# Performance work log

Measured on AMD Instinct MI355X. Metric: run time of the kernel, lower is better.

The kernel has to match this reference:

```python
import jax, jax.numpy as jnp
import numpy as np

N, E, R, D, DEPTH = 50000, 800000, 1000, 128, 2


def setup_inputs() -> dict:
    key = jax.random.key(0)
    ks = jax.random.split(key, 6)
    features = jax.random.normal(ks[0], (N, D), jnp.float32)
    rel_emb = jax.random.normal(ks[1], (R, D), jnp.float32)
    # adj coalesced by row (torch coalesce sorts indices; values stay aligned)
    src = jnp.sort(jax.random.randint(ks[2], (E,), 0, N))
    dst = jax.random.randint(ks[3], (E,), 0, N)
    adj = jnp.stack([src, dst]).astype(jnp.int64)
    # one relation per triple: row index = triple id, col = relation id
    r_index = jnp.stack([jnp.arange(E), jax.random.randint(ks[4], (E,), 0, R)]).astype(jnp.int64)
    r_val = jax.random.uniform(ks[5], (E,), jnp.float32)
    attn_kernels = jax.random.normal(jax.random.fold_in(key, 7), (DEPTH, D), jnp.float32) * 0.1
    return {"features": features, "rel_emb": rel_emb, "adj": adj, "r_index": r_index,
            "r_val": r_val, "triple_size": E, "rel_size": R, "node_size": N,
            "attn_kernels": attn_kernels}


def _layer(features, rel_emb, adj, r_index, r_val, triple_size, node_size, attn_k):
    row = adj[0]
    neighs = features[adj[1]]                                   # [E, D] gather
    # sparse.mm(tri_rel, rel_emb): sum_j r_val * rel_emb[col] per triple row
    tri_rel = jax.ops.segment_sum(r_val[:, None] * rel_emb[r_index[1]],
                                  r_index[0], num_segments=triple_size)  # [E, D]
    nrm = jnp.linalg.norm(tri_rel, axis=1, keepdims=True)
    tri_rel = tri_rel / jnp.maximum(nrm, 1e-12)                 # F.normalize(p=2)
    # Householder-style reflection
    neighs = neighs - 2.0 * jnp.sum(neighs * tri_rel, axis=1, keepdims=True) * tri_rel
    att = tri_rel @ attn_k                                      # [E]
    # sparse row-wise softmax over edges grouped by destination row
    m = jax.ops.segment_max(att, row, num_segments=node_size)
    e = jnp.exp(att - m[row])
    s = jax.ops.segment_sum(e, row, num_segments=node_size)
    att = e / s[row]
    new_features = jax.ops.segment_sum(neighs * att[:, None], row,
                                       num_segments=node_size)  # [N, D] scatter
    return jnp.tanh(new_features)


def reference(features, rel_emb, adj, r_index, r_val, triple_size, rel_size, node_size, attn_kernels):
    features = jnp.tanh(features)
    outputs = [features]
    for l in range(attn_kernels.shape[0]):
        features = _layer(features, rel_emb, adj, r_index, r_val,
                          triple_size, node_size, attn_kernels[l])
        outputs.append(features)
    return jnp.concatenate(outputs, axis=-1)                    # [N, D*(depth+1)]
```

## Files before the change

### kernel.cpp

```cpp
#include <hip/hip_runtime.h>
#include <hip/hip_bf16.h>
#include <math.h>

#define N_NODES   50000
#define N_EDGES   800000
#define N_REL     1000
#define DIM       128
#define DEPTH_L   2
#define OUT_STRIDE (DIM * (DEPTH_L + 1))

#define TANH0_BLOCKS  ((N_NODES * 32) / 256)
#define EINFO_BLOCKS  ((N_EDGES + 255) / 256)

typedef _Float16 h2 __attribute__((ext_vector_type(2)));

#if defined(__has_builtin)
#if __has_builtin(__builtin_amdgcn_fdot2)
#define FDOT2(a, b, c) __builtin_amdgcn_fdot2((a), (b), (c), false)
#endif
#endif
#ifndef FDOT2
#define FDOT2(a, b, c) ((c) + (float)(a).x * (float)(b).x + (float)(a).y * (float)(b).y)
#endif

__device__ __forceinline__ float fast_tanh(float x) {
    float cx = fminf(fmaxf(x, -15.f), 15.f);
    float e = __expf(2.f * cx);
    return (e - 1.f) * __frcp_rn(e + 1.f);
}

__global__ __launch_bounds__(64) void prep_rel_kernel(
    const float* __restrict__ rel_emb,
    const float* __restrict__ attn_k,
    _Float16* __restrict__ rhat,
    float* __restrict__ er0, float* __restrict__ er1)
{
    int r = blockIdx.x;
    int lane = threadIdx.x;
    if (r == N_REL) {
        rhat[(size_t)r * DIM + lane]      = (_Float16)0.f;
        rhat[(size_t)r * DIM + lane + 64] = (_Float16)0.f;
        if (lane == 0) { er0[N_REL] = 1.f; er1[N_REL] = 1.f; }
        return;
    }
    float v0 = rel_emb[r * DIM + lane];
    float v1 = rel_emb[r * DIM + lane + 64];
    float ss = v0 * v0 + v1 * v1;
    #pragma unroll
    for (int o = 32; o >= 1; o >>= 1) ss += __shfl_xor(ss, o);
    float inv = 1.0f / fmaxf(sqrtf(ss), 1e-12f);
    float t0 = v0 * inv, t1 = v1 * inv;
    rhat[(size_t)r * DIM + lane]      = (_Float16)t0;
    rhat[(size_t)r * DIM + lane + 64] = (_Float16)t1;
    #pragma unroll
    for (int l = 0; l < DEPTH_L; ++l) {
        float d = t0 * attn_k[l * DIM + lane] + t1 * attn_k[l * DIM + lane + 64];
        #pragma unroll
        for (int o = 32; o >= 1; o >>= 1) d += __shfl_xor(d, o);
        if (lane == 0) {
            if (l == 0) er0[r] = __expf(d); else er1[r] = __expf(d);
        }
    }
}

__global__ __launch_bounds__(256) void rowptr_kernel(
    const int* __restrict__ src, int* __restrict__ rp,
    float* __restrict__ s0, float* __restrict__ s1)
{
    int n = blockIdx.x * blockDim.x + threadIdx.x;
    if (n > N_NODES) return;
    int lo = 0, hi = N_EDGES;
    while (lo < hi) {
        int mid = (lo + hi) >> 1;
        if (src[mid] < n) lo = mid + 1; else hi = mid;
    }
    rp[n] = lo;
    if (n < N_NODES) { s0[n] = 0.f; s1[n] = 0.f; }
}

__global__ __launch_bounds__(256) void aux_fused_kernel(
    const float* __restrict__ feat, float* __restrict__ out,
    _Float16* __restrict__ fs0,
    const int* __restrict__ src, const int* __restrict__ dst,
    const int* __restrict__ relid, const float* __restrict__ rval,
    const float* __restrict__ er0, const float* __restrict__ er1,
    float* __restrict__ s0, float* __restrict__ s1,
    uint2* __restrict__ einfo2)
{
    if (blockIdx.x < TANH0_BLOCKS) {
        int i = blockIdx.x * 256 + threadIdx.x;
        int n = i >> 5;
        int j = i & 31;
        float4 v = reinterpret_cast<const float4*>(feat + (size_t)n * DIM)[j];
        float4 o;
        o.x = fast_tanh(v.x); o.y = fast_tanh(v.y);
        o.z = fast_tanh(v.z); o.w = fast_tanh(v.w);
        reinterpret_cast<float4*>(out + (size_t)n * OUT_STRIDE)[j] = o;
        h2 p0; p0.x = (_Float16)o.x; p0.y = (_Float16)o.y;
        h2 p1; p1.x = (_Float16)o.z; p1.y = (_Float16)o.w;
        uint2 u;
        u.x = __builtin_bit_cast(unsigned, p0);
        u.y = __builtin_bit_cast(unsigned, p1);
        reinterpret_cast<uint2*>(fs0 + (size_t)n * DIM)[j] = u;
        return;
    }

    int e = (blockIdx.x - TANH0_BLOCKS) * 256 + threadIdx.x;
    if (e >= N_EDGES) return;
    int lane = threadIdx.x & 63;
    int sn = src[e];
    int r = (rval[e] == 0.f) ? N_REL : relid[e];
    float x0 = er0[r], x1 = er1[r];

    h2 ep; ep.x = (_Float16)x0; ep.y = (_Float16)x1;
    einfo2[e] = make_uint2((unsigned)dst[e] | ((unsigned)r << 16),
                           __builtin_bit_cast(unsigned, ep));

    #pragma unroll
    for (int off = 1; off < 64; off <<= 1) {
        float y0 = __shfl_up(x0, off);
        float y1 = __shfl_up(x1, off);
        int   sp = __shfl_up(sn, off);
        if (lane >= off && sp == sn) { x0 += y0; x1 += y1; }
    }
    int snext = __shfl_down(sn, 1);
    bool lastlane = (lane == 63) || (e == N_EDGES - 1) || (snext != sn);
    if (lastlane) {
        atomicAdd(&s0[sn], x0);
        atomicAdd(&s1[sn], x1);
    }
}

template<int L>
__global__ __launch_bounds__(128) void layer_fused_kernel(
    const _Float16* __restrict__ fs_in,
    float* __restrict__ fout,
    _Float16* __restrict__ fs_out,
    const uint2* __restrict__ einfo2,
    const int* __restrict__ rp,
    const float* __restrict__ s_l,
    const _Float16* __restrict__ rhat)
{
    int wid  = threadIdx.x >> 6;
    int lane = threadIdx.x & 63;
    int node = blockIdx.x * 2 + wid;
    if (node >= N_NODES) return;
    int start = rp[node], end = rp[node + 1];
    int g = lane >> 3;
    int q = lane & 7;

    float inv_s = 1.0f / s_l[node];

    const char* fbase = (const char*)fs_in + 32 * q;
    const char* tbase = (const char*)rhat  + 32 * q;
    int g0 = (lane >> 3) & 1, g1 = (lane >> 4) & 1, g2 = (lane >> 5) & 1;

    h2 a2[8];
    #pragma unroll
    for (int i = 0; i < 8; ++i) { a2[i].x = (_Float16)0.f; a2[i].y = (_Float16)0.f; }

    if (start < end) {
        int deg = end - start;
        bool small = (deg <= 64);
        unsigned eix = 0, eiy = 0;
        if (small) {
            int lc = start + lane; if (lc > end - 1) lc = end - 1;
            uint2 et = einfo2[lc];
            eix = et.x; eiy = et.y;
        }

        auto LOADC = [&](int e0, uint4& h0, uint4& h1, uint4& t0, uint4& t1,
                         float& w) {
            unsigned ax, ay;
            if (small) {
                int slot = e0 - start + g;
                ax = __shfl(eix, slot);
                ay = __shfl(eiy, slot);
            } else {
                int ec = e0 + g; if (ec > end - 1) ec = end - 1;
                uint2 et = einfo2[ec];
                ax = et.x; ay = et.y;
            }
            bool valid = (e0 + g < end);
            h0 = make_uint4(0u, 0u, 0u, 0u); h1 = h0; t0 = h0; t1 = h0;
            if (valid) {
                unsigned dn = ax & 0xffffu, rl = ax >> 16;
                const uint4* hp = reinterpret_cast<const uint4*>(fbase + (size_t)dn * 256);
                const uint4* tp = reinterpret_cast<const uint4*>(tbase + (size_t)rl * 256);
                h0 = hp[0]; h1 = hp[1];
                t0 = tp[0]; t1 = tp[1];
            }
            h2 ep = __builtin_bit_cast(h2, ay);
            float er = (float)((L == 0) ? ep.x : ep.y);
            w = valid ? er * inv_s : 0.f;
        };

        auto COMPUTEC = [&](uint4 h0, uint4 h1, uint4 t0, uint4 t1, float wf) {
            h2 hh[8], tt[8];
            hh[0] = __builtin_bit_cast(h2, h0.x); hh[1] = __builtin_bit_cast(h2, h0.y);
            hh[2] = __builtin_bit_cast(h2, h0.z); hh[3] = __builtin_bit_cast(h2, h0.w);
            hh[4] = __builtin_bit_cast(h2, h1.x); hh[5] = __builtin_bit_cast(h2, h1.y);
            hh[6] = __builtin_bit_cast(h2, h1.z); hh[7] = __builtin_bit_cast(h2, h1.w);
            tt[0] = __builtin_bit_cast(h2, t0.x); tt[1] = __builtin_bit_cast(h2, t0.y);
            tt[2] = __builtin_bit_cast(h2, t0.z); tt[3] = __builtin_bit_cast(h2, t0.w);
            tt[4] = __builtin_bit_cast(h2, t1.x); tt[5] = __builtin_bit_cast(h2, t1.y);
            tt[6] = __builtin_bit_cast(h2, t1.z); tt[7] = __builtin_bit_cast(h2, t1.w);
            float d0 = 0.f, d1 = 0.f;
            #pragma unroll
            for (int p = 0; p < 8; p += 2) {
                d0 = FDOT2(hh[p],     tt[p],     d0);
                d1 = FDOT2(hh[p + 1], tt[p + 1], d1);
            }
            float d = d0 + d1;
            d += __shfl_xor(d, 1);
            d += __shfl_xor(d, 2);
            d += __shfl_xor(d, 4);
            float cf = -2.f * wf * d;
            _Float16 wh  = (_Float16)wf;
            _Float16 cfh = (_Float16)cf;
            h2 wv; wv.x = wh;  wv.y = wh;
            h2 cv; cv.x = cfh; cv.y = cfh;
            #pragma unroll
            for (int p = 0; p < 8; ++p) {
                a2[p] = hh[p] * wv + a2[p];
                a2[p] = tt[p] * cv + a2[p];
            }
        };

        uint4 hA0, hA1, tA0, tA1; float wA;
        uint4 hB0, hB1, tB0, tB1; float wB;
        LOADC(start, hA0, hA1, tA0, tA1, wA);
        int e = start;
        while (true) {
            int e2 = e + 8;
            bool moreB = (e2 < end);
            if (moreB) LOADC(e2, hB0, hB1, tB0, tB1, wB);
            __builtin_amdgcn_sched_barrier(0);
            COMPUTEC(hA0, hA1, tA0, tA1, wA);
            e = e2;
            if (!moreB) break;
            int e3 = e + 8;
            bool moreA = (e3 < end);
            if (moreA) LOADC(e3, hA0, hA1, tA0, tA1, wA);
            __builtin_amdgcn_sched_barrier(0);
            COMPUTEC(hB0, hB1, tB0, tB1, wB);
            e = e3;
            if (!moreA) break;
        }
    }

    h2 b1[4];
    #pragma unroll
    for (int k = 0; k < 4; ++k) {
        h2 keep = g0 ? a2[2*k + 1] : a2[2*k];
        h2 send = g0 ? a2[2*k] : a2[2*k + 1];
        unsigned su = __shfl_xor(__builtin_bit_cast(unsigned, send), 8);
        b1[k] = keep + __builtin_bit_cast(h2, su);
    }
    h2 b2[2];
    #pragma unroll
    for (int m = 0; m < 2; ++m) {
        h2 keep = g1 ? b1[2*m + 1] : b1[2*m];
        h2 send = g1 ? b1[2*m] : b1[2*m + 1];
        unsigned su = __shfl_xor(__builtin_bit_cast(unsigned, send), 16);
        b2[m] = keep + __builtin_bit_cast(h2, su);
    }
    h2 c;
    {
        h2 keep = g2 ? b2[1] : b2[0];
        h2 send = g2 ? b2[0] : b2[1];
        unsigned su = __shfl_xor(__builtin_bit_cast(unsigned, send), 32);
        c = keep + __builtin_bit_cast(h2, su);
    }

    float y0 = fast_tanh((float)c.x), y1 = fast_tanh((float)c.y);
    int dimo = 16 * q + 2 * g;
    *reinterpret_cast<float2*>(fout + (size_t)node * OUT_STRIDE + dimo)
        = make_float2(y0, y1);
    if (L == 0) {
        h2 pr; pr.x = (_Float16)y0; pr.y = (_Float16)y1;
        *reinterpret_cast<h2*>(fs_out + (size_t)node * DIM + dimo) = pr;
    }
}

extern "C" void kernel_launch(void* const* d_in, const int* in_sizes, int n_in,
                              void* d_out, int out_size, void* d_ws, size_t ws_size,
                              hipStream_t stream)
{
    const float* features = (const float*)d_in[0];
    const float* rel_emb  = (const float*)d_in[1];
    const int*   adj      = (const int*)d_in[2];
    const int*   r_index  = (const int*)d_in[3];
    const float* r_val    = (const float*)d_in[4];
    const float* attn_k   = (const float*)d_in[8];
    float* out = (float*)d_out;

    const int* src   = adj;
    const int* dst   = adj + N_EDGES;
    const int* relid = r_index + N_EDGES;

    char* base = (char*)d_ws;
    _Float16* rhat = (_Float16*)base;
    float*    er0  = (float*)(base + 256256);
    float*    er1  = (float*)(base + 260264);
    int*      rp   = (int*)(base + 264272);
    float*    s0   = (float*)(base + 464288);
    float*    s1   = (float*)(base + 664288);
    uint2*    einfo2 = (uint2*)(base + 864288);
    _Float16* fs0  = (_Float16*)(base + 864288 + (size_t)N_EDGES * 8);
    _Float16* fs1  = fs0 + (size_t)N_NODES * DIM;

    prep_rel_kernel<<<N_REL + 1, 64, 0, stream>>>(rel_emb, attn_k, rhat, er0, er1);
    rowptr_kernel<<<(N_NODES + 1 + 255) / 256, 256, 0, stream>>>(src, rp, s0, s1);
    aux_fused_kernel<<<TANH0_BLOCKS + EINFO_BLOCKS, 256, 0, stream>>>(
        features, out, fs0, src, dst, relid, r_val, er0, er1, s0, s1, einfo2);

    layer_fused_kernel<0><<<(N_NODES + 1) / 2, 128, 0, stream>>>(
        fs0, out + 1 * DIM, fs1, einfo2, rp, s0, rhat);
    layer_fused_kernel<1><<<(N_NODES + 1) / 2, 128, 0, stream>>>(
        fs1, out + 2 * DIM, fs0, einfo2, rp, s1, rhat);
}
```

Baseline: 111.9 us.

## Process two nodes per wave in layer kernel and merge prep kernels

```diff
diff --git a/kernel.cpp b/kernel.cpp
--- a/kernel.cpp
+++ b/kernel.cpp
@@ -11,6 +11,8 @@
 
 #define TANH0_BLOCKS  ((N_NODES * 32) / 256)
 #define EINFO_BLOCKS  ((N_EDGES + 255) / 256)
+#define PREP_BLOCKS   ((N_REL + 1 + 3) / 4)
+#define RP_BLOCKS     ((N_NODES + 1 + 255) / 256)
 
 typedef _Float16 h2 __attribute__((ext_vector_type(2)));
 
@@ -29,45 +31,47 @@
     return (e - 1.f) * __frcp_rn(e + 1.f);
 }
 
-__global__ __launch_bounds__(64) void prep_rel_kernel(
+__global__ __launch_bounds__(256) void prep_kernel(
     const float* __restrict__ rel_emb,
     const float* __restrict__ attn_k,
     _Float16* __restrict__ rhat,
-    float* __restrict__ er0, float* __restrict__ er1)
-{
-    int r = blockIdx.x;
-    int lane = threadIdx.x;
-    if (r == N_REL) {
-        rhat[(size_t)r * DIM + lane]      = (_Float16)0.f;
-        rhat[(size_t)r * DIM + lane + 64] = (_Float16)0.f;
-        if (lane == 0) { er0[N_REL] = 1.f; er1[N_REL] = 1.f; }
-        return;
-    }
-    float v0 = rel_emb[r * DIM + lane];
-    float v1 = rel_emb[r * DIM + lane + 64];
-    float ss = v0 * v0 + v1 * v1;
-    #pragma unroll
-    for (int o = 32; o >= 1; o >>= 1) ss += __shfl_xor(ss, o);
-    float inv = 1.0f / fmaxf(sqrtf(ss), 1e-12f);
-    float t0 = v0 * inv, t1 = v1 * inv;
-    rhat[(size_t)r * DIM + lane]      = (_Float16)t0;
-    rhat[(size_t)r * DIM + lane + 64] = (_Float16)t1;
-    #pragma unroll
-    for (int l = 0; l < DEPTH_L; ++l) {
-        float d = t0 * attn_k[l * DIM + lane] + t1 * attn_k[l * DIM + lane + 64];
-        #pragma unroll
-        for (int o = 32; o >= 1; o >>= 1) d += __shfl_xor(d, o);
-        if (lane == 0) {
-            if (l == 0) er0[r] = __expf(d); else er1[r] = __expf(d);
-        }
-    }
-}
-
-__global__ __launch_bounds__(256) void rowptr_kernel(
+    float* __restrict__ er0, float* __restrict__ er1,
     const int* __restrict__ src, int* __restrict__ rp,
     float* __restrict__ s0, float* __restrict__ s1)
 {
-    int n = blockIdx.x * blockDim.x + threadIdx.x;
+    if (blockIdx.x < PREP_BLOCKS) {
+        int wid  = threadIdx.x >> 6;
+        int lane = threadIdx.x & 63;
+        int r = blockIdx.x * 4 + wid;
+        if (r > N_REL) return;
+        if (r == N_REL) {
+            rhat[(size_t)r * DIM + lane]      = (_Float16)0.f;
+            rhat[(size_t)r * DIM + lane + 64] = (_Float16)0.f;
+            if (lane == 0) { er0[N_REL] = 1.f; er1[N_REL] = 1.f; }
+            return;
+        }
+        float v0 = rel_emb[r * DIM + lane];
+        float v1 = rel_emb[r * DIM + lane + 64];
+        float ss = v0 * v0 + v1 * v1;
+        #pragma unroll
+        for (int o = 32; o >= 1; o >>= 1) ss += __shfl_xor(ss, o);
+        float inv = 1.0f / fmaxf(sqrtf(ss), 1e-12f);
+        float t0 = v0 * inv, t1 = v1 * inv;
+        rhat[(size_t)r * DIM + lane]      = (_Float16)t0;
+        rhat[(size_t)r * DIM + lane + 64] = (_Float16)t1;
+        #pragma unroll
+        for (int l = 0; l < DEPTH_L; ++l) {
+            float d = t0 * attn_k[l * DIM + lane] + t1 * attn_k[l * DIM + lane + 64];
+            #pragma unroll
+            for (int o = 32; o >= 1; o >>= 1) d += __shfl_xor(d, o);
+            if (lane == 0) {
+                if (l == 0) er0[r] = __expf(d); else er1[r] = __expf(d);
+            }
+        }
+        return;
+    }
+
+    int n = (blockIdx.x - PREP_BLOCKS) * 256 + threadIdx.x;
     if (n > N_NODES) return;
     int lo = 0, hi = N_EDGES;
     while (lo < hi) {
@@ -143,21 +147,27 @@
 {
     int wid  = threadIdx.x >> 6;
     int lane = threadIdx.x & 63;
-    int node = blockIdx.x * 2 + wid;
-    if (node >= N_NODES) return;
-    int start = rp[node], end = rp[node + 1];
+    int wave = blockIdx.x * 2 + wid;
+    int n0 = wave * 2;
+    if (n0 >= N_NODES) return;
+    int n1 = n0 + 1;
+    int start = rp[n0], mid = rp[n0 + 1], end = rp[n0 + 2];
+
+    float is0 = 1.0f / s_l[n0];
+    float is1 = 1.0f / s_l[n1];
+
     int g = lane >> 3;
     int q = lane & 7;
-
-    float inv_s = 1.0f / s_l[node];
-
     const char* fbase = (const char*)fs_in + 32 * q;
     const char* tbase = (const char*)rhat  + 32 * q;
     int g0 = (lane >> 3) & 1, g1 = (lane >> 4) & 1, g2 = (lane >> 5) & 1;
 
-    h2 a2[8];
+    h2 aA[8], aB[8];
     #pragma unroll
-    for (int i = 0; i < 8; ++i) { a2[i].x = (_Float16)0.f; a2[i].y = (_Float16)0.f; }
+    for (int i = 0; i < 8; ++i) {
+        aA[i].x = (_Float16)0.f; aA[i].y = (_Float16)0.f;
+        aB[i].x = (_Float16)0.f; aB[i].y = (_Float16)0.f;
+    }
 
     if (start < end) {
         int deg = end - start;
@@ -192,10 +202,25 @@
             }
             h2 ep = __builtin_bit_cast(h2, ay);
             float er = (float)((L == 0) ? ep.x : ep.y);
-            w = valid ? er * inv_s : 0.f;
+            float isv = (e0 + g >= mid) ? is1 : is0;
+            w = valid ? er * isv : 0.f;
         };
 
-        auto COMPUTEC = [&](uint4 h0, uint4 h1, uint4 t0, uint4 t1, float wf) {
+        auto ACC = [&](h2 (&acc)[8], float wf, float cf,
+                       const h2 (&hh)[8], const h2 (&tt)[8]) {
+            _Float16 wh  = (_Float16)wf;
+            _Float16 cfh = (_Float16)cf;
+            h2 wv; wv.x = wh;  wv.y = wh;
+            h2 cv; cv.x = cfh; cv.y = cfh;
+            #pragma unroll
+            for (int p = 0; p < 8; ++p) {
+                acc[p] = hh[p] * wv + acc[p];
+                acc[p] = tt[p] * cv + acc[p];
+            }
+        };
+
+        auto DOCHUNK = [&](int e0, uint4 h0, uint4 h1, uint4 t0, uint4 t1,
+                           float wf) {
             h2 hh[8], tt[8];
             hh[0] = __builtin_bit_cast(h2, h0.x); hh[1] = __builtin_bit_cast(h2, h0.y);
             hh[2] = __builtin_bit_cast(h2, h0.z); hh[3] = __builtin_bit_cast(h2, h0.w);
@@ -216,14 +241,18 @@
             d += __shfl_xor(d, 2);
             d += __shfl_xor(d, 4);
             float cf = -2.f * wf * d;
-            _Float16 wh  = (_Float16)wf;
-            _Float16 cfh = (_Float16)cf;
-            h2 wv; wv.x = wh;  wv.y = wh;
-            h2 cv; cv.x = cfh; cv.y = cfh;
-            #pragma unroll
-            for (int p = 0; p < 8; ++p) {
-                a2[p] = hh[p] * wv + a2[p];
-                a2[p] = tt[p] * cv + a2[p];
+
+            int realEnd = (e0 + 8 < end) ? (e0 + 8) : end;
+            if (realEnd <= mid) {
+                ACC(aA, wf, cf, hh, tt);
+            } else if (e0 >= mid) {
+                ACC(aB, wf, cf, hh, tt);
+            } else {
+                bool ma = (e0 + g < mid);
+                float wfa = ma ? wf : 0.f, cfa = ma ? cf : 0.f;
+                float wfb = ma ? 0.f : wf, cfb = ma ? 0.f : cf;
+                ACC(aA, wfa, cfa, hh, tt);
+                ACC(aB, wfb, cfb, hh, tt);
             }
         };
 
@@ -236,51 +265,54 @@
             bool moreB = (e2 < end);
             if (moreB) LOADC(e2, hB0, hB1, tB0, tB1, wB);
             __builtin_amdgcn_sched_barrier(0);
-            COMPUTEC(hA0, hA1, tA0, tA1, wA);
-            e = e2;
+            DOCHUNK(e, hA0, hA1, tA0, tA1, wA);
             if (!moreB) break;
-            int e3 = e + 8;
+            int e3 = e2 + 8;
             bool moreA = (e3 < end);
             if (moreA) LOADC(e3, hA0, hA1, tA0, tA1, wA);
             __builtin_amdgcn_sched_barrier(0);
-            COMPUTEC(hB0, hB1, tB0, tB1, wB);
+            DOCHUNK(e2, hB0, hB1, tB0, tB1, wB);
             e = e3;
             if (!moreA) break;
         }
     }
 
-    h2 b1[4];
-    #pragma unroll
-    for (int k = 0; k < 4; ++k) {
-        h2 keep = g0 ? a2[2*k + 1] : a2[2*k];
-        h2 send = g0 ? a2[2*k] : a2[2*k + 1];
-        unsigned su = __shfl_xor(__builtin_bit_cast(unsigned, send), 8);
-        b1[k] = keep + __builtin_bit_cast(h2, su);
-    }
-    h2 b2[2];
-    #pragma unroll
-    for (int m = 0; m < 2; ++m) {
-        h2 keep = g1 ? b1[2*m + 1] : b1[2*m];
-        h2 send = g1 ? b1[2*m] : b1[2*m + 1];
-        unsigned su = __shfl_xor(__builtin_bit_cast(unsigned, send), 16);
-        b2[m] = keep + __builtin_bit_cast(h2, su);
-    }
-    h2 c;
-    {
-        h2 keep = g2 ? b2[1] : b2[0];
-        h2 send = g2 ? b2[0] : b2[1];
-        unsigned su = __shfl_xor(__builtin_bit_cast(unsigned, send), 32);
-        c = keep + __builtin_bit_cast(h2, su);
-    }
-
-    float y0 = fast_tanh((float)c.x), y1 = fast_tanh((float)c.y);
-    int dimo = 16 * q + 2 * g;
-    *reinterpret_cast<float2*>(fout + (size_t)node * OUT_STRIDE + dimo)
-        = make_float2(y0, y1);
-    if (L == 0) {
-        h2 pr; pr.x = (_Float16)y0; pr.y = (_Float16)y1;
-        *reinterpret_cast<h2*>(fs_out + (size_t)node * DIM + dimo) = pr;
-    }
+    auto FOLDW = [&](h2 (&a2)[8], int node) {
+        h2 b1[4];
+        #pragma unroll
+        for (int k = 0; k < 4; ++k) {
+            h2 keep = g0 ? a2[2*k + 1] : a2[2*k];
+            h2 send = g0 ? a2[2*k] : a2[2*k + 1];
+            unsigned su = __shfl_xor(__builtin_bit_cast(unsigned, send), 8);
+            b1[k] = keep + __builtin_bit_cast(h2, su);
+        }
+        h2 b2[2];
+        #pragma unroll
+        for (int m = 0; m < 2; ++m) {
+            h2 keep = g1 ? b1[2*m + 1] : b1[2*m];
+            h2 send = g1 ? b1[2*m] : b1[2*m + 1];
+            unsigned su = __shfl_xor(__builtin_bit_cast(unsigned, send), 16);
+            b2[m] = keep + __builtin_bit_cast(h2, su);
+        }
+        h2 c;
+        {
+            h2 keep = g2 ? b2[1] : b2[0];
+            h2 send = g2 ? b2[0] : b2[1];
+            unsigned su = __shfl_xor(__builtin_bit_cast(unsigned, send), 32);
+            c = keep + __builtin_bit_cast(h2, su);
+        }
+        float y0 = fast_tanh((float)c.x), y1 = fast_tanh((float)c.y);
+        int dimo = 16 * q + 2 * g;
+        *reinterpret_cast<float2*>(fout + (size_t)node * OUT_STRIDE + dimo)
+            = make_float2(y0, y1);
+        if (L == 0) {
+            h2 pr; pr.x = (_Float16)y0; pr.y = (_Float16)y1;
+            *reinterpret_cast<h2*>(fs_out + (size_t)node * DIM + dimo) = pr;
+        }
+    };
+
+    FOLDW(aA, n0);
+    FOLDW(aB, n1);
 }
 
 extern "C" void kernel_launch(void* const* d_in, const int* in_sizes, int n_in,
@@ -310,13 +342,13 @@
     _Float16* fs0  = (_Float16*)(base + 864288 + (size_t)N_EDGES * 8);
     _Float16* fs1  = fs0 + (size_t)N_NODES * DIM;
 
-    prep_rel_kernel<<<N_REL + 1, 64, 0, stream>>>(rel_emb, attn_k, rhat, er0, er1);
-    rowptr_kernel<<<(N_NODES + 1 + 255) / 256, 256, 0, stream>>>(src, rp, s0, s1);
+    prep_kernel<<<PREP_BLOCKS + RP_BLOCKS, 256, 0, stream>>>(
+        rel_emb, attn_k, rhat, er0, er1, src, rp, s0, s1);
     aux_fused_kernel<<<TANH0_BLOCKS + EINFO_BLOCKS, 256, 0, stream>>>(
         features, out, fs0, src, dst, relid, r_val, er0, er1, s0, s1, einfo2);
 
-    layer_fused_kernel<0><<<(N_NODES + 1) / 2, 128, 0, stream>>>(
+    layer_fused_kernel<0><<<(N_NODES / 2 + 1) / 2, 128, 0, stream>>>(
         fs0, out + 1 * DIM, fs1, einfo2, rp, s0, rhat);
-    layer_fused_kernel<1><<<(N_NODES + 1) / 2, 128, 0, stream>>>(
+    layer_fused_kernel<1><<<(N_NODES / 2 + 1) / 2, 128, 0, stream>>>(
         fs1, out + 2 * DIM, fs0, einfo2, rp, s1, rhat);
 }
```

New measurement: 109.4 us, median of 2. -2.2%, faster.
